# Optimization experiments

Hardware: AMD Instinct MI355X
Metric: run time of the kernel (lower is better)

## Reference

```python
import jax, jax.numpy as jnp
import numpy as np

EMBED_DIM = 2048
NUM_HEADS = 16
HEAD_DIM = EMBED_DIM // NUM_HEADS


def setup_inputs() -> dict:
    key = jax.random.key(0)
    k1, k2, k3, k4 = jax.random.split(key, 4)
    x = jax.random.normal(k1, (4, 2048, EMBED_DIM), dtype=jnp.float32)
    # torch nn.Linear weight shape: [out_features, in_features]
    W_qkv = jax.random.normal(k2, (3 * EMBED_DIM, EMBED_DIM), dtype=jnp.float32) * (EMBED_DIM ** -0.5)
    W_out = jax.random.normal(k3, (EMBED_DIM, EMBED_DIM), dtype=jnp.float32) * (EMBED_DIM ** -0.5)
    b_out = jax.random.normal(k4, (EMBED_DIM,), dtype=jnp.float32) * 0.01
    return {"x": x, "W_qkv": W_qkv, "W_out": W_out, "b_out": b_out}


def reference(x, W_qkv, W_out, b_out):
    B, S, E = x.shape
    H, D = NUM_HEADS, HEAD_DIM
    qkv = jnp.einsum('bse,fe->bsf', x, W_qkv)            # [B,S,3E]
    q, k, v = jnp.split(qkv, 3, axis=-1)
    # [B,S,E] -> [B,H,S,D]
    q = q.reshape(B, S, H, D).transpose(0, 2, 1, 3)
    k = k.reshape(B, S, H, D).transpose(0, 2, 1, 3)
    v = v.reshape(B, S, H, D).transpose(0, 2, 1, 3)
    scale = D ** -0.5
    scores = jnp.einsum('bhqd,bhkd->bhqk', q, k) * scale  # [B,H,S,S]
    attn = jax.nn.softmax(scores, axis=-1)
    out = jnp.einsum('bhqk,bhkd->bhqd', attn, v)          # [B,H,S,D]
    out = out.transpose(0, 2, 1, 3).reshape(B, S, E)
    return jnp.einsum('bse,fe->bsf', out, W_out) + b_out
```

## Files before the change

kernel.cpp:

```cpp
#include <hip/hip_runtime.h>
#include <stdint.h>
#include <stddef.h>

#define BATCH 4
#define SEQ   2048
#define EDIM  2048
#define NH    16
#define HD    128
#define MTOT  (BATCH*SEQ)

#define QSCALE (0.08838834764831845f * 1.4426950408889634f)

typedef __bf16 bf16_t;
typedef __attribute__((ext_vector_type(8))) __bf16 bf16x8;
typedef __attribute__((ext_vector_type(4))) __bf16 bf16x4;
typedef __attribute__((ext_vector_type(4))) float f32x4;
typedef __attribute__((ext_vector_type(16))) float f32x16;
typedef __attribute__((ext_vector_type(2))) unsigned int uint32x2;

#define GLD16(l, g) __builtin_amdgcn_global_load_lds( \
    (const uint32_t __attribute__((address_space(1)))*)(g), \
    (uint32_t __attribute__((address_space(3)))*)(l), 16, 0, 0)

#define RAW_BARRIER()  asm volatile("s_barrier" ::: "memory")
#define WAITCNT_VM(n)  asm volatile("s_waitcnt vmcnt(" #n ")" ::: "memory")

__global__ void cast_bf16_kernel(const float* __restrict__ in,
                                 bf16_t* __restrict__ out, int n4) {
    int i = blockIdx.x * blockDim.x + threadIdx.x;
    if (i < n4) {
        float4 v = ((const float4*)in)[i];
        bf16x4 o = { (__bf16)v.x, (__bf16)v.y, (__bf16)v.z, (__bf16)v.w };
        ((bf16x4*)out)[i] = o;
    }
}

#define STAGE_A(dst, src, bm_, k0_, h) do { \
  _Pragma("unroll") \
  for (int i_ = 0; i_ < 2; i_++) { \
    int idx_ = i_*512 + tid; \
    int lr_ = idx_ >> 3, c_ = idx_ & 7; \
    int gr_ = (lr_ & 63) + ((lr_ & 64) << 1) + (h)*64; \
    GLD16(&(dst)[gr_*64 + c_*8], \
          (src) + ((bm_) + gr_)*(long)K + (k0_) + ((c_ ^ (gr_ & 7)) * 8)); \
  } } while (0)

#define STAGE_B(dst, src, bn_, k0_, h) do { \
  _Pragma("unroll") \
  for (int i_ = 0; i_ < 2; i_++) { \
    int idx_ = i_*512 + tid; \
    int lr_ = idx_ >> 3, c_ = idx_ & 7; \
    int gr_ = (lr_ & 31) + ((lr_ >> 5) << 6) + (h)*32; \
    GLD16(&(dst)[gr_*64 + c_*8], \
          (src) + ((bn_) + gr_)*(long)K + (k0_) + ((c_ ^ (gr_ & 7)) * 8)); \
  } } while (0)

#define READ_A(MB) do { \
  _Pragma("unroll") for (int mt_ = 0; mt_ < 4; mt_++) \
  _Pragma("unroll") for (int kk_ = 0; kk_ < 2; kk_++) \
    a[mt_][kk_] = *(const bf16x8*)&Ac[(wm + (MB)*64 + mt_*16 + l15)*64 + \
                                      (((kk_*4 + quad) ^ (l15 & 7)) * 8)]; } while (0)

#define READ_B(NB) do { \
  _Pragma("unroll") for (int nt_ = 0; nt_ < 2; nt_++) \
  _Pragma("unroll") for (int kk_ = 0; kk_ < 2; kk_++) \
    b[(NB)*2 + nt_][kk_] = *(const bf16x8*)&Bc[(wn + (NB)*32 + nt_*16 + l15)*64 + \
                                               (((kk_*4 + quad) ^ (l15 & 7)) * 8)]; } while (0)

#define MFMA_Q(MB, NB) do { \
  __builtin_amdgcn_s_setprio(1); \
  _Pragma("unroll") for (int mt_ = 0; mt_ < 4; mt_++) \
  _Pragma("unroll") for (int nt_ = 0; nt_ < 2; nt_++) \
  _Pragma("unroll") for (int kk_ = 0; kk_ < 2; kk_++) \
    acc[(MB)*4 + mt_][(NB)*2 + nt_] = __builtin_amdgcn_mfma_f32_16x16x32_bf16( \
        a[mt_][kk_], b[(NB)*2 + nt_][kk_], acc[(MB)*4 + mt_][(NB)*2 + nt_], 0, 0, 0); \
  __builtin_amdgcn_s_setprio(0); } while (0)

template<int EPI>
__global__ __launch_bounds__(512, 2)
void gemm_nt(const bf16_t* __restrict__ A, const bf16_t* __restrict__ B,
             int M, int N, int K,
             float* __restrict__ outf, const float* __restrict__ bias,
             bf16_t* __restrict__ qb, bf16_t* __restrict__ kb,
             bf16_t* __restrict__ vb)
{
    __shared__ bf16_t SA[2][256*64];
    __shared__ bf16_t SB[2][256*64];
    const int tid  = threadIdx.x;
    const int lane = tid & 63;
    const int l15  = lane & 15;
    const int quad = lane >> 4;
    const int wave = tid >> 6;
    const int wm = (wave >> 2) * 128;
    const int wn = (wave & 3) * 64;

    const int nbx = M >> 8;
    const int cpx = gridDim.x >> 3;
    const int bid = blockIdx.x;
    const int swz = (bid & 7) * cpx + (bid >> 3);
    const long bm = (long)(swz % nbx) * 256;
    const long bn = (long)(swz / nbx) * 256;

    f32x4 acc[8][4] = {};
    bf16x8 a[4][2], b[4][2];

    const int NT = K >> 6;

    STAGE_A(SA[0], A, bm, 0, 0);
    STAGE_B(SB[0], B, bn, 0, 0);
    STAGE_B(SB[0], B, bn, 0, 1);
    STAGE_A(SA[0], A, bm, 0, 1);
    WAITCNT_VM(4);
    RAW_BARRIER();

    for (int t = 0; t < NT; t++) {
        bf16_t* const Ac = SA[t & 1];
        bf16_t* const Bc = SB[t & 1];
        bf16_t* const An = SA[(t & 1) ^ 1];
        bf16_t* const Bn = SB[(t & 1) ^ 1];
        const long kn = (t + 1 == NT) ? 0 : (long)(t + 1) * 64;

        READ_A(0); READ_B(0);
        STAGE_A(An, A, bm, kn, 0);
        WAITCNT_VM(4);
        RAW_BARRIER();
        MFMA_Q(0, 0);
        RAW_BARRIER();
        READ_B(1);
        STAGE_B(Bn, B, bn, kn, 0);
        WAITCNT_VM(4);
        RAW_BARRIER();
        MFMA_Q(0, 1);
        RAW_BARRIER();
        READ_A(1);
        STAGE_B(Bn, B, bn, kn, 1);
        RAW_BARRIER();
        MFMA_Q(1, 1);
        RAW_BARRIER();
        STAGE_A(An, A, bm, kn, 1);
        WAITCNT_VM(4);
        RAW_BARRIER();
        MFMA_Q(1, 0);
        RAW_BARRIER();
    }

    if (EPI == 0) {
#pragma unroll
        for (int nt = 0; nt < 4; nt++) {
            int colg = (int)bn + wn + nt*16 + l15;
            int which = colg >> 11;
            int e = colg & 2047;
            int h = e >> 7, d = e & 127;
#pragma unroll
            for (int mt = 0; mt < 8; mt++) {
#pragma unroll
                for (int r = 0; r < 4; r++) {
                    int rowg = (int)bm + wm + mt*16 + quad*4 + r;
                    int bb = rowg >> 11, s = rowg & 2047;
                    long bh = (long)bb*NH + h;
                    if (which == 0)
                        qb[(bh*SEQ + s)*HD + d] = (__bf16)(acc[mt][nt][r] * QSCALE);
                    else if (which == 1)
                        kb[(bh*SEQ + s)*HD + d] = (__bf16)acc[mt][nt][r];
                    else
                        vb[(bh*HD + d)*SEQ + s] = (__bf16)acc[mt][nt][r];
                }
            }
        }
    } else {
#pragma unroll
        for (int nt = 0; nt < 4; nt++) {
            int colg = (int)bn + wn + nt*16 + l15;
            float bv = bias[colg];
#pragma unroll
            for (int mt = 0; mt < 8; mt++)
#pragma unroll
                for (int r = 0; r < 4; r++) {
                    int rowg = (int)bm + wm + mt*16 + quad*4 + r;
                    outf[(long)rowg*EDIM + colg] = acc[mt][nt][r] + bv;
                }
        }
    }
}

__device__ __forceinline__ void pswap(uint32_t& x, uint32_t& y) {
    uint32x2 r = __builtin_amdgcn_permlane32_swap(x, y, false, false);
    x = r[0]; y = r[1];
}
__device__ __forceinline__ uint32_t pkbf16(float a, float b) {
    union { uint32_t u; __bf16 h[2]; } w;
    w.h[0] = (__bf16)a; w.h[1] = (__bf16)b;
    return w.u;
}
__device__ __forceinline__ float xswap_max(float v) {
    union { float f; uint32_t u; } a, b;
    a.f = v; b.f = v;
    pswap(a.u, b.u);
    return fmaxf(a.f, b.f);
}
__device__ __forceinline__ float xswap_add(float v) {
    union { float f; uint32_t u; } a, b;
    a.f = v; b.f = v;
    pswap(a.u, b.u);
    return a.f + b.f;
}

template<int B>
__device__ __forceinline__ bf16x8 mkfrag(f32x16 p) {
    uint32_t w0 = pkbf16(p[B+0], p[B+1]);
    uint32_t w2 = pkbf16(p[B+4], p[B+5]);
    pswap(w0, w2);
    uint32_t w1 = pkbf16(p[B+2], p[B+3]);
    uint32_t w3 = pkbf16(p[B+6], p[B+7]);
    pswap(w1, w3);
    union { uint32_t u[4]; bf16x8 v; } r;
    r.u[0] = w0; r.u[1] = w1; r.u[2] = w2; r.u[3] = w3;
    return r.v;
}

__global__ __launch_bounds__(512, 2)
void attn_kernel(const bf16_t* __restrict__ qb, const bf16_t* __restrict__ kb,
                 const bf16_t* __restrict__ vb, bf16_t* __restrict__ ob)
{
    __shared__ bf16_t SM[32768];
    bf16_t* const K0 = SM;
    bf16_t* const K1 = SM + 8192;
    bf16_t* const V0 = SM + 16384;
    bf16_t* const V1 = SM + 24576;

    const int tid  = threadIdx.x;
    const int lane = tid & 63;
    const int l31  = lane & 31;
    const int l15  = lane & 15;
    const int l7   = lane & 7;
    const int hi   = lane >> 5;
    const int warp = tid >> 6;

    const int bh = blockIdx.x & 63;
    const int q0 = (blockIdx.x >> 6) * 256;
    const int b  = bh >> 4;
    const int h  = bh & 15;

    const bf16_t* kg0 = kb + (long)bh*SEQ*HD;
    const bf16_t* vg0 = vb + (long)bh*HD*SEQ;

    bf16x8 qf[8];
    {
        const bf16_t* qg = qb + ((long)bh*SEQ + q0 + warp*32 + l31)*HD + hi*8;
#pragma unroll
        for (int ds = 0; ds < 8; ds++)
            qf[ds] = *(const bf16x8*)(qg + ds*16);
    }

#pragma unroll
    for (int i = 0; i < 2; i++) {
        int lin = i*4096 + tid*8;
        { int row = lin >> 7, c = (lin >> 3) & 15;
          GLD16(&K0[lin], kg0 + (long)row*HD + ((c ^ (row & 15)) * 8)); }
        { int row = lin >> 6, c = (lin >> 3) & 7;
          GLD16(&V0[lin], vg0 + (long)row*SEQ + ((c ^ (row & 7)) * 8)); }
    }

    f32x16 oacc[4] = {};
    float m = -1e30f, lsum = 0.f;

    const int NT = SEQ / 64;
    for (int t = 0; t < NT; t++) {
        bf16_t* const Kc = (t & 1) ? K1 : K0;
        bf16_t* const Vc = (t & 1) ? V1 : V0;
        bf16_t* const Kn = (t & 1) ? K0 : K1;
        bf16_t* const Vn = (t & 1) ? V0 : V1;

        RAW_BARRIER();
        {
            int tn = (t + 1 == NT) ? 0 : t + 1;
            const bf16_t* kg = kg0 + (long)tn*64*HD;
            const bf16_t* vg = vg0 + tn*64;
#pragma unroll
            for (int i = 0; i < 2; i++) {
                int lin = i*4096 + tid*8;
                { int row = lin >> 7, c = (lin >> 3) & 15;
                  GLD16(&Kn[lin], kg + (long)row*HD + ((c ^ (row & 15)) * 8)); }
                { int row = lin >> 6, c = (lin >> 3) & 7;
                  GLD16(&Vn[lin], vg + (long)row*SEQ + ((c ^ (row & 7)) * 8)); }
            }
        }
        WAITCNT_VM(4);
        RAW_BARRIER();

        f32x16 p0 = {}, p1 = {};
        __builtin_amdgcn_s_setprio(1);
#pragma unroll
        for (int ds = 0; ds < 8; ds++) {
            const int sc = ((ds*2 + hi) ^ l15) * 8;
            bf16x8 kf0 = *(const bf16x8*)&Kc[l31*128 + sc];
            bf16x8 kf1 = *(const bf16x8*)&Kc[(32 + l31)*128 + sc];
            p0 = __builtin_amdgcn_mfma_f32_32x32x16_bf16(kf0, qf[ds], p0, 0, 0, 0);
            p1 = __builtin_amdgcn_mfma_f32_32x32x16_bf16(kf1, qf[ds], p1, 0, 0, 0);
        }
        __builtin_amdgcn_s_setprio(0);

        float mx;
        {
            float tm[8];
#pragma unroll
            for (int r = 0; r < 8; r++)
                tm[r] = fmaxf(fmaxf(p0[r], p0[r+8]), fmaxf(p1[r], p1[r+8]));
#pragma unroll
            for (int s2 = 4; s2 > 0; s2 >>= 1)
#pragma unroll
                for (int r = 0; r < s2; r++) tm[r] = fmaxf(tm[r], tm[r+s2]);
            mx = xswap_max(tm[0]);
        }
        float mo = m;
        float mn = fmaxf(mo, mx);
        m = mn;
        if (__any(mn > mo)) {
            float av = exp2f(mo - mn);
            lsum *= av;
#pragma unroll
            for (int d = 0; d < 4; d++)
#pragma unroll
                for (int r = 0; r < 16; r++) oacc[d][r] *= av;
        }
#pragma unroll
        for (int r = 0; r < 16; r++) p0[r] = exp2f(p0[r] - mn);
#pragma unroll
        for (int r = 0; r < 16; r++) p1[r] = exp2f(p1[r] - mn);
        {
            float ts[8];
#pragma unroll
            for (int r = 0; r < 8; r++)
                ts[r] = (p0[r] + p0[r+8]) + (p1[r] + p1[r+8]);
#pragma unroll
            for (int s2 = 4; s2 > 0; s2 >>= 1)
#pragma unroll
                for (int r = 0; r < s2; r++) ts[r] += ts[r+s2];
            lsum += xswap_add(ts[0]);
        }

        bf16x8 pf0 = mkfrag<0>(p0);
        bf16x8 pf1 = mkfrag<8>(p0);
        bf16x8 pf2 = mkfrag<0>(p1);
        bf16x8 pf3 = mkfrag<8>(p1);
        __builtin_amdgcn_s_setprio(1);
#pragma unroll
        for (int d = 0; d < 4; d++) {
            bf16x8 vf0 = *(const bf16x8*)&Vc[(d*32 + l31)*64 + (((0 + hi) ^ l7) * 8)];
            oacc[d] = __builtin_amdgcn_mfma_f32_32x32x16_bf16(vf0, pf0, oacc[d], 0, 0, 0);
            bf16x8 vf1 = *(const bf16x8*)&Vc[(d*32 + l31)*64 + (((2 + hi) ^ l7) * 8)];
            oacc[d] = __builtin_amdgcn_mfma_f32_32x32x16_bf16(vf1, pf1, oacc[d], 0, 0, 0);
            bf16x8 vf2 = *(const bf16x8*)&Vc[(d*32 + l31)*64 + (((4 + hi) ^ l7) * 8)];
            oacc[d] = __builtin_amdgcn_mfma_f32_32x32x16_bf16(vf2, pf2, oacc[d], 0, 0, 0);
            bf16x8 vf3 = *(const bf16x8*)&Vc[(d*32 + l31)*64 + (((6 + hi) ^ l7) * 8)];
            oacc[d] = __builtin_amdgcn_mfma_f32_32x32x16_bf16(vf3, pf3, oacc[d], 0, 0, 0);
        }
        __builtin_amdgcn_s_setprio(0);
    }

    {
        float inv = 1.0f / lsum;
        long obase = ((long)b*SEQ + q0 + warp*32 + l31)*EDIM + h*HD + hi*8;
#pragma unroll
        for (int d = 0; d < 4; d++) {
            f32x16 o;
#pragma unroll
            for (int r = 0; r < 16; r++) o[r] = oacc[d][r] * inv;
            bf16x8 f0 = mkfrag<0>(o);
            bf16x8 f1 = mkfrag<8>(o);
            *(bf16x8*)&ob[obase + d*32]      = f0;
            *(bf16x8*)&ob[obase + d*32 + 16] = f1;
        }
    }
}

extern "C" void kernel_launch(void* const* d_in, const int* in_sizes, int n_in,
                              void* d_out, int out_size, void* d_ws, size_t ws_size,
                              hipStream_t stream) {
    const float* x    = (const float*)d_in[0];
    const float* wqkv = (const float*)d_in[1];
    const float* wout = (const float*)d_in[2];
    const float* bout = (const float*)d_in[3];
    float* out = (float*)d_out;

    char* w = (char*)d_ws;
    bf16_t* xb    = (bf16_t*)w; w += (size_t)MTOT*EDIM*2;
    bf16_t* wqkvb = (bf16_t*)w; w += (size_t)3*EDIM*EDIM*2;
    bf16_t* woutb = (bf16_t*)w; w += (size_t)EDIM*EDIM*2;
    bf16_t* qbuf  = (bf16_t*)w; w += (size_t)MTOT*EDIM*2;
    bf16_t* kbuf  = (bf16_t*)w; w += (size_t)MTOT*EDIM*2;
    bf16_t* vbuf  = (bf16_t*)w; w += (size_t)MTOT*EDIM*2;
    bf16_t* attnb = (bf16_t*)w; w += (size_t)MTOT*EDIM*2;

    cast_bf16_kernel<<<MTOT*EDIM/1024, 256, 0, stream>>>(x, xb, MTOT*EDIM/4);
    cast_bf16_kernel<<<3*EDIM*EDIM/1024, 256, 0, stream>>>(wqkv, wqkvb, 3*EDIM*EDIM/4);
    cast_bf16_kernel<<<EDIM*EDIM/1024, 256, 0, stream>>>(wout, woutb, EDIM*EDIM/4);

    gemm_nt<0><<<dim3((MTOT/256)*(3*EDIM/256)), 512, 0, stream>>>(
        xb, wqkvb, MTOT, 3*EDIM, EDIM, nullptr, nullptr, qbuf, kbuf, vbuf);

    attn_kernel<<<dim3(512), 512, 0, stream>>>(qbuf, kbuf, vbuf, attnb);

    gemm_nt<1><<<dim3((MTOT/256)*(EDIM/256)), 512, 0, stream>>>(
        attnb, woutb, MTOT, EDIM, EDIM, out, bout, nullptr, nullptr, nullptr);
}
```

Baseline: 691.5 us.

## Restructure GEMM main loop pipeline and use XCD-aware block mapping

The GEMM k-loop is rescheduled so both B half-tiles are staged earlier, with deeper vmcnt waits, and four of the eight barriers per iteration are removed. Split b0/b1 register arrays keep B fragments live across the quadrants, so the last MFMA quadrant reuses b0 without rereading shared memory. Block-to-tile mapping changes so each XCD gets a contiguous range of M tiles, aiming for better L2 locality. Removing barriers risks LDS read/write races between waves, and the extra live registers may raise register pressure.

```diff
diff --git a/kernel.cpp b/kernel.cpp
--- a/kernel.cpp
+++ b/kernel.cpp
@@ -61,19 +61,19 @@
     a[mt_][kk_] = *(const bf16x8*)&Ac[(wm + (MB)*64 + mt_*16 + l15)*64 + \
                                       (((kk_*4 + quad) ^ (l15 & 7)) * 8)]; } while (0)
 
-#define READ_B(NB) do { \
+#define READ_B(arr, NB) do { \
   _Pragma("unroll") for (int nt_ = 0; nt_ < 2; nt_++) \
   _Pragma("unroll") for (int kk_ = 0; kk_ < 2; kk_++) \
-    b[(NB)*2 + nt_][kk_] = *(const bf16x8*)&Bc[(wn + (NB)*32 + nt_*16 + l15)*64 + \
-                                               (((kk_*4 + quad) ^ (l15 & 7)) * 8)]; } while (0)
-
-#define MFMA_Q(MB, NB) do { \
+    arr[nt_][kk_] = *(const bf16x8*)&Bc[(wn + (NB)*32 + nt_*16 + l15)*64 + \
+                                        (((kk_*4 + quad) ^ (l15 & 7)) * 8)]; } while (0)
+
+#define MFMA_Q(MB, NB, arr) do { \
   __builtin_amdgcn_s_setprio(1); \
   _Pragma("unroll") for (int mt_ = 0; mt_ < 4; mt_++) \
   _Pragma("unroll") for (int nt_ = 0; nt_ < 2; nt_++) \
   _Pragma("unroll") for (int kk_ = 0; kk_ < 2; kk_++) \
     acc[(MB)*4 + mt_][(NB)*2 + nt_] = __builtin_amdgcn_mfma_f32_16x16x32_bf16( \
-        a[mt_][kk_], b[(NB)*2 + nt_][kk_], acc[(MB)*4 + mt_][(NB)*2 + nt_], 0, 0, 0); \
+        a[mt_][kk_], arr[nt_][kk_], acc[(MB)*4 + mt_][(NB)*2 + nt_], 0, 0, 0); \
   __builtin_amdgcn_s_setprio(0); } while (0)
 
 template<int EPI>
@@ -94,15 +94,14 @@
     const int wm = (wave >> 2) * 128;
     const int wn = (wave & 3) * 64;
 
-    const int nbx = M >> 8;
-    const int cpx = gridDim.x >> 3;
-    const int bid = blockIdx.x;
-    const int swz = (bid & 7) * cpx + (bid >> 3);
-    const long bm = (long)(swz % nbx) * 256;
-    const long bn = (long)(swz / nbx) * 256;
+    const int MC  = (M >> 8) >> 3;
+    const int xcd = blockIdx.x & 7;
+    const int j   = blockIdx.x >> 3;
+    const long bm = (long)(xcd * MC + (j % MC)) * 256;
+    const long bn = (long)(j / MC) * 256;
 
     f32x4 acc[8][4] = {};
-    bf16x8 a[4][2], b[4][2];
+    bf16x8 a[4][2], b0[2][2], b1[2][2];
 
     const int NT = K >> 6;
 
@@ -120,28 +119,24 @@
         bf16_t* const Bn = SB[(t & 1) ^ 1];
         const long kn = (t + 1 == NT) ? 0 : (long)(t + 1) * 64;
 
-        READ_A(0); READ_B(0);
+        READ_A(0); READ_B(b0, 0);
         STAGE_A(An, A, bm, kn, 0);
+        STAGE_B(Bn, B, bn, kn, 0);
+        WAITCNT_VM(6);
+        RAW_BARRIER();
+        MFMA_Q(0, 0, b0);
+        READ_B(b1, 1);
+        STAGE_B(Bn, B, bn, kn, 1);
+        WAITCNT_VM(6);
+        RAW_BARRIER();
+        MFMA_Q(0, 1, b1);
+        READ_A(1);
+        STAGE_A(An, A, bm, kn, 1);
+        RAW_BARRIER();
+        MFMA_Q(1, 1, b1);
         WAITCNT_VM(4);
         RAW_BARRIER();
-        MFMA_Q(0, 0);
-        RAW_BARRIER();
-        READ_B(1);
-        STAGE_B(Bn, B, bn, kn, 0);
-        WAITCNT_VM(4);
-        RAW_BARRIER();
-        MFMA_Q(0, 1);
-        RAW_BARRIER();
-        READ_A(1);
-        STAGE_B(Bn, B, bn, kn, 1);
-        RAW_BARRIER();
-        MFMA_Q(1, 1);
-        RAW_BARRIER();
-        STAGE_A(An, A, bm, kn, 1);
-        WAITCNT_VM(4);
-        RAW_BARRIER();
-        MFMA_Q(1, 0);
-        RAW_BARRIER();
+        MFMA_Q(1, 0, b0);
     }
 
     if (EPI == 0) {
```

Measured after the change: 627.2 us. 1.1x faster.
